# Kernel tuning notes

Hardware: AMD Instinct MI355X
Metric: run time of the kernel (lower is better)

Reference implementation:

```python
import jax, jax.numpy as jnp
import numpy as np

B, S, H = 2, 2048, 2048
N_HEADS, N_KV, HEAD_DIM = 16, 8, 128
EPS = 1e-6
ROPE_THETA = 1e6


def _rms_norm(x, w, eps=EPS):
    # per-head RMSNorm over last dim (head_dim), computed in fp32
    xf = x.astype(jnp.float32)
    var = jnp.mean(xf * xf, axis=-1, keepdims=True)
    return (w * (xf * jax.lax.rsqrt(var + eps))).astype(x.dtype)


def _rotate_half(x):
    x1, x2 = jnp.split(x, 2, axis=-1)
    return jnp.concatenate((-x2, x1), axis=-1)


def setup_inputs() -> dict:
    key = jax.random.key(0)
    ks = jax.random.split(key, 6)
    hidden_states = jax.random.normal(ks[0], (B, S, H), dtype=jnp.float32)
    # RoPE tables: [B, S, head_dim]
    inv_freq = 1.0 / (ROPE_THETA ** (np.arange(0, HEAD_DIM, 2, dtype=np.float32) / HEAD_DIM))
    pos = np.arange(S, dtype=np.float32)
    freqs = np.outer(pos, inv_freq)                      # [S, head_dim/2]
    emb = np.concatenate([freqs, freqs], axis=-1)        # [S, head_dim]
    cos = jnp.broadcast_to(jnp.asarray(np.cos(emb)), (B, S, HEAD_DIM))
    sin = jnp.broadcast_to(jnp.asarray(np.sin(emb)), (B, S, HEAD_DIM))
    # additive causal mask [B, 1, S, S]
    causal = jnp.triu(jnp.full((S, S), -1e9, dtype=jnp.float32), k=1)
    attention_mask = jnp.broadcast_to(causal[None, None], (B, 1, S, S))
    scale = 0.02
    Wq = jax.random.normal(ks[1], (N_HEADS * HEAD_DIM, H), dtype=jnp.float32) * scale
    Wk = jax.random.normal(ks[2], (N_KV * HEAD_DIM, H), dtype=jnp.float32) * scale
    Wv = jax.random.normal(ks[3], (N_KV * HEAD_DIM, H), dtype=jnp.float32) * scale
    Wo = jax.random.normal(ks[4], (H, N_HEADS * HEAD_DIM), dtype=jnp.float32) * scale
    q_norm_w = jnp.ones((HEAD_DIM,), dtype=jnp.float32)
    k_norm_w = jnp.ones((HEAD_DIM,), dtype=jnp.float32)
    return dict(hidden_states=hidden_states, cos=cos, sin=sin,
                attention_mask=attention_mask, Wq=Wq, Wk=Wk, Wv=Wv, Wo=Wo,
                q_norm_w=q_norm_w, k_norm_w=k_norm_w)


def reference(hidden_states, cos, sin, attention_mask, Wq, Wk, Wv, Wo, q_norm_w, k_norm_w):
    b, s, _ = hidden_states.shape
    scaling = HEAD_DIM ** -0.5
    n_rep = N_HEADS // N_KV
    # QKV projections (torch Linear: x @ W.T), split into heads
    q = jnp.einsum('bsh,dh->bsd', hidden_states, Wq).reshape(b, s, N_HEADS, HEAD_DIM)
    k = jnp.einsum('bsh,dh->bsd', hidden_states, Wk).reshape(b, s, N_KV, HEAD_DIM)
    v = jnp.einsum('bsh,dh->bsd', hidden_states, Wv).reshape(b, s, N_KV, HEAD_DIM)
    # per-head QK RMSNorm, then [B, H, S, D]
    q = _rms_norm(q, q_norm_w).transpose(0, 2, 1, 3)
    k = _rms_norm(k, k_norm_w).transpose(0, 2, 1, 3)
    v = v.transpose(0, 2, 1, 3)
    # RoPE (cos/sin unsqueezed over head dim)
    c = cos[:, None, :, :]
    sn = sin[:, None, :, :]
    q = q * c + _rotate_half(q) * sn
    k = k * c + _rotate_half(k) * sn
    # GQA: repeat kv heads
    k = jnp.repeat(k, n_rep, axis=1)
    v = jnp.repeat(v, n_rep, axis=1)
    # eager attention: materialize full [B, H, S, S] scores
    attn_weights = jnp.einsum('bhqd,bhkd->bhqk', q, k) * scaling + attention_mask
    attn_weights = jax.nn.softmax(attn_weights.astype(jnp.float32), axis=-1).astype(q.dtype)
    attn_output = jnp.einsum('bhqk,bhkd->bhqd', attn_weights, v)
    attn_output = attn_output.transpose(0, 2, 1, 3).reshape(b, s, N_HEADS * HEAD_DIM)
    attn_output = jnp.einsum('bsd,hd->bsh', attn_output, Wo)
    return attn_output, attn_weights
```

## Files before the change

### kernel.cpp

```cpp
#include <hip/hip_runtime.h>
#include <stdint.h>

typedef unsigned short u16;
typedef __attribute__((ext_vector_type(8))) short bf16x8;
typedef __attribute__((ext_vector_type(4))) float f32x4;
typedef __attribute__((ext_vector_type(8))) unsigned short u16x8;

#define SCALE_LOG2E 0.12751743007633614f

__device__ __forceinline__ u16 f2bf(float x){
  uint32_t u = __float_as_uint(x);
  u += 0x7FFFu + ((u >> 16) & 1u);
  return (u16)(u >> 16);
}
__device__ __forceinline__ float bf2f(u16 h){
  return __uint_as_float(((uint32_t)h) << 16);
}
__device__ __forceinline__ void gload16(const void* g, void* l){
  __builtin_amdgcn_global_load_lds((const __attribute__((address_space(1))) void*)g,
                                   (__attribute__((address_space(3))) void*)l, 16, 0, 0);
}

__global__ __launch_bounds__(256) void k_cvt5(
    const float* __restrict__ s0, u16* __restrict__ d0,
    const float* __restrict__ s1, u16* __restrict__ d1,
    const float* __restrict__ s2, u16* __restrict__ d2,
    const float* __restrict__ s3, u16* __restrict__ d3,
    const float* __restrict__ s4, u16* __restrict__ d4)
{
  int b = blockIdx.x;
  const float* s; u16* d; int off;
  if      (b < 8192)  { s=s0; d=d0; off=b; }
  else if (b < 12288) { s=s1; d=d1; off=b-8192; }
  else if (b < 14336) { s=s2; d=d2; off=b-12288; }
  else if (b < 16384) { s=s3; d=d3; off=b-14336; }
  else                { s=s4; d=d4; off=b-16384; }
  size_t i = ((size_t)off * 256 + threadIdx.x) * 4;
  float4 v = *(const float4*)(s + i);
  ushort4 o;
  o.x = f2bf(v.x); o.y = f2bf(v.y); o.z = f2bf(v.z); o.w = f2bf(v.w);
  *(ushort4*)(d + i) = o;
}

#define STAGE_UNIT(PTR, ROWOFF, BUF, TENS, KS, T1) do{ \
  _Pragma("unroll") \
  for(int jj=0;jj<2;jj++){ \
    int rs_ = wid*32 + jj*16 + (lane>>2); \
    int kp_ = (lane&3) ^ ((rs_>>1)&3); \
    gload16((PTR) + (size_t)((ROWOFF)+rs_)*K + (size_t)(T1)*64 + (KS)*32 + kp_*8, \
            &lds[BUF][TENS][KS][(wid*2+jj)*512]); \
  }}while(0)

#define FRAG(BASE, ROW) (*(const bf16x8*)((BASE) + (ROW)*32 + ((c_ ^ (((ROW)>>1)&3))<<3)))

__global__ __launch_bounds__(512,2) void k_gemm256(
    const u16* __restrict__ A, const u16* __restrict__ Bw, void* __restrict__ Cout,
    int N, int K, int ldc, int out_f32)
{
  __shared__ u16 lds[2][2][2][256*32];
  const int tid = threadIdx.x, wid = tid>>6, lane = tid&63;
  const int nbn = N >> 8;
  const int cpx = gridDim.x >> 3;
  const int bid = (blockIdx.x & 7)*cpx + (blockIdx.x >> 3);
  const int bm = bid / nbn, bn = bid % nbn;
  const int m0 = bm<<8, n0 = bn<<8;
  const int wm = wid>>2, wn = wid&3;
  const int c_ = lane>>4, rl = lane&15;

  f32x4 acc[8][4];
  f32x4 zero4 = {0.f,0.f,0.f,0.f};
#pragma unroll
  for (int i=0;i<8;i++)
#pragma unroll
    for (int j=0;j<4;j++) acc[i][j] = zero4;

  STAGE_UNIT(A,  m0, 0, 0, 0, 0);
  STAGE_UNIT(Bw, n0, 0, 1, 0, 0);
  STAGE_UNIT(A,  m0, 0, 0, 1, 0);
  STAGE_UNIT(Bw, n0, 0, 1, 1, 0);

  const int nt = K >> 6;
#pragma unroll 2
  for (int t=0; t<nt; ++t) {
    const int cur = t&1, nxt = cur^1;
    const bool pf = (t+1 < nt);
    const u16* Ab0 = lds[cur][0][0];
    const u16* Bb0 = lds[cur][1][0];
    const u16* Ab1 = lds[cur][0][1];
    const u16* Bb1 = lds[cur][1][1];
    bf16x8 af[4], bf[4];

    asm volatile("s_waitcnt vmcnt(4)" ::: "memory");
    __builtin_amdgcn_s_barrier();
    asm volatile("" ::: "memory");
#pragma unroll
    for (int j=0;j<4;j++) bf[j] = FRAG(Bb0, wn*64 + j*16 + rl);
#pragma unroll
    for (int i=0;i<4;i++) af[i] = FRAG(Ab0, wm*128 + i*16 + rl);
    if (pf) STAGE_UNIT(A, m0, nxt, 0, 0, t+1);
    __builtin_amdgcn_s_setprio(1);
#pragma unroll
    for (int i=0;i<4;i++)
#pragma unroll
      for (int j=0;j<4;j++)
        acc[i][j] = __builtin_amdgcn_mfma_f32_16x16x32_bf16(af[i], bf[j], acc[i][j], 0,0,0);
    __builtin_amdgcn_s_setprio(0);
    __builtin_amdgcn_s_barrier();
    asm volatile("" ::: "memory");

#pragma unroll
    for (int i=0;i<4;i++) af[i] = FRAG(Ab0, wm*128 + (i+4)*16 + rl);
    if (pf) STAGE_UNIT(Bw, n0, nxt, 1, 0, t+1);
    __builtin_amdgcn_s_setprio(1);
#pragma unroll
    for (int i=0;i<4;i++)
#pragma unroll
      for (int j=0;j<4;j++)
        acc[i+4][j] = __builtin_amdgcn_mfma_f32_16x16x32_bf16(af[i], bf[j], acc[i+4][j], 0,0,0);
    __builtin_amdgcn_s_setprio(0);
    __builtin_amdgcn_s_barrier();
    asm volatile("" ::: "memory");

    if (pf) { asm volatile("s_waitcnt vmcnt(4)" ::: "memory"); }
    else    { asm volatile("s_waitcnt vmcnt(0)" ::: "memory"); }
    __builtin_amdgcn_s_barrier();
    asm volatile("" ::: "memory");
#pragma unroll
    for (int j=0;j<4;j++) bf[j] = FRAG(Bb1, wn*64 + j*16 + rl);
#pragma unroll
    for (int i=0;i<4;i++) af[i] = FRAG(Ab1, wm*128 + i*16 + rl);
    if (pf) STAGE_UNIT(A, m0, nxt, 0, 1, t+1);
    __builtin_amdgcn_s_setprio(1);
#pragma unroll
    for (int i=0;i<4;i++)
#pragma unroll
      for (int j=0;j<4;j++)
        acc[i][j] = __builtin_amdgcn_mfma_f32_16x16x32_bf16(af[i], bf[j], acc[i][j], 0,0,0);
    __builtin_amdgcn_s_setprio(0);
    __builtin_amdgcn_s_barrier();
    asm volatile("" ::: "memory");

#pragma unroll
    for (int i=0;i<4;i++) af[i] = FRAG(Ab1, wm*128 + (i+4)*16 + rl);
    if (pf) STAGE_UNIT(Bw, n0, nxt, 1, 1, t+1);
    __builtin_amdgcn_s_setprio(1);
#pragma unroll
    for (int i=0;i<4;i++)
#pragma unroll
      for (int j=0;j<4;j++)
        acc[i+4][j] = __builtin_amdgcn_mfma_f32_16x16x32_bf16(af[i], bf[j], acc[i+4][j], 0,0,0);
    __builtin_amdgcn_s_setprio(0);
    __builtin_amdgcn_s_barrier();
    asm volatile("" ::: "memory");
  }

  const int r0 = m0 + wm*128 + ((lane>>4)<<2);
  const int c0 = n0 + wn*64 + rl;
  if (out_f32) {
    float* C = (float*)Cout;
#pragma unroll
    for (int i=0;i<8;i++)
#pragma unroll
      for (int j=0;j<4;j++)
#pragma unroll
        for (int r=0;r<4;r++)
          C[(size_t)(r0 + i*16 + r)*ldc + (c0 + j*16)] = acc[i][j][r];
  } else {
    u16* C = (u16*)Cout;
#pragma unroll
    for (int i=0;i<8;i++)
#pragma unroll
      for (int j=0;j<4;j++)
#pragma unroll
        for (int r=0;r<4;r++)
          C[(size_t)(r0 + i*16 + r)*ldc + (c0 + j*16)] = f2bf(acc[i][j][r]);
  }
}

__global__ __launch_bounds__(256) void k_normrope(
    u16* __restrict__ qkv, const float* __restrict__ cosb, const float* __restrict__ sinb,
    const float* __restrict__ qw, const float* __restrict__ kw)
{
  const int tid = threadIdx.x, lane = tid&63;
  const int task = blockIdx.x*4 + (tid>>6);
  int bs, col; const float* w;
  if (task < 65536) { bs = task >> 4; col = (task & 15)*128; w = qw; }
  else { int t2 = task - 65536; bs = t2 >> 3; col = 2048 + (t2 & 7)*128; w = kw; }
  u16* row = qkv + (size_t)bs*4096 + col;
  float x0 = bf2f(row[lane]), x1 = bf2f(row[lane+64]);
  float ss = x0*x0 + x1*x1;
#pragma unroll
  for (int m=1; m<64; m<<=1) ss += __shfl_xor(ss, m, 64);
  float rn = rsqrtf(ss*(1.0f/128.0f) + 1e-6f);
  const float* cp = cosb + (size_t)bs*128;
  const float* sp = sinb + (size_t)bs*128;
  float q0 = x0*rn*w[lane], q1 = x1*rn*w[lane+64];
  float o0 = q0*cp[lane]    - q1*sp[lane];
  float o1 = q1*cp[lane+64] + q0*sp[lane+64];
  row[lane]    = f2bf(o0);
  row[lane+64] = f2bf(o1);
}

__global__ __launch_bounds__(256) void k_vtrans(const u16* __restrict__ qkv, u16* __restrict__ vt)
{
  const int bid = blockIdx.x;
  const int dt = bid & 1, st = (bid>>1)&31, kvh = (bid>>6)&7, b = bid>>9;
  __shared__ u16 tile[64][72];
  const int tid = threadIdx.x;
  const int rr = tid >> 3, c = (tid & 7) * 8;
  const u16* src = qkv + ((size_t)(b*2048 + st*64))*4096 + 3072 + kvh*128 + dt*64;
#pragma unroll
  for (int p=0;p<2;p++){
    int sl = p*32 + rr;
    u16x8 v = *(const u16x8*)(src + (size_t)sl*4096 + c);
#pragma unroll
    for (int e=0;e<8;e++) tile[sl][c+e] = v[e];
  }
  __syncthreads();
  u16* dst = vt + ((size_t)((b*8+kvh)*128 + dt*64))*2048 + st*64;
#pragma unroll
  for (int p=0;p<2;p++){
    int dl = p*32 + rr;
    u16x8 o;
#pragma unroll
    for (int e=0;e<8;e++) o[e] = tile[c+e][dl];
    *(u16x8*)(dst + (size_t)dl*2048 + c) = o;
  }
}

#define STAGE_K(T, DSTBUF) do { \
  _Pragma("unroll") \
  for (int i_=0;i_<4;i_++){ \
    int r_ = wv*16 + i_*4 + (lane>>4); \
    int cs_ = (lane&15) ^ (r_&7); \
    gload16(Kb + (size_t)((T)*64 + r_)*4096 + cs_*8, (DSTBUF) + (wv*4+i_)*512); \
  } } while(0)

#define STAGE_V(T, DSTBUF) do { \
  _Pragma("unroll") \
  for (int i_=0;i_<4;i_++){ \
    int d_ = wv*32 + i_*8 + (lane>>3); \
    int cs_ = (lane&7) ^ (d_&7); \
    gload16(Vb + (size_t)d_*2048 + (T)*64 + cs_*8, (DSTBUF) + (wv*4+i_)*512); \
  } } while(0)

#define COMPUTE_S(SACC, KBUF) do { \
  _Pragma("unroll") \
  for (int ks_=0;ks_<4;ks_++){ \
    bf16x8 bfr_[4]; \
    _Pragma("unroll") \
    for (int ns_=0;ns_<4;ns_++){ \
      int n_ = ns_*16 + (lane&15); \
      int sl_ = (ks_*4 + (lane>>4)) ^ (n_&7); \
      bfr_[ns_] = *(const bf16x8*)((KBUF) + n_*128 + sl_*8); \
    } \
    _Pragma("unroll") \
    for (int ms_=0;ms_<2;ms_++) \
      _Pragma("unroll") \
      for (int ns_=0;ns_<4;ns_++) \
        SACC[ms_][ns_] = __builtin_amdgcn_mfma_f32_16x16x32_bf16(qf[ms_][ks_], bfr_[ns_], SACC[ms_][ns_], 0,0,0); \
  } } while(0)

__global__ __launch_bounds__(256) void k_attn(
    const u16* __restrict__ qkv, const u16* __restrict__ vt,
    float* __restrict__ probs, u16* __restrict__ attn_o)
{
  __shared__ u16 lK[2][64*128];
  __shared__ u16 lV[2][128*64];
  __shared__ u16 lP[4][32*64];
  const int tid = threadIdx.x, wv = tid>>6, lane = tid&63;
  const int bid = blockIdx.x;
  const int r9 = bid >> 5;
  const int qt = (r9 < 8) ? (15 - r9) : (r9 - 8);
  const int bh = bid & 31;
  const int h = bh & 15, b = bh >> 4;
  const int kvh = h>>1;
  const int q0 = qt<<7;
  const u16* Qb = qkv + (size_t)b*2048*4096 + h*128;
  const u16* Kb = qkv + (size_t)b*2048*4096 + 2048 + kvh*128;
  const u16* Vb = vt + (size_t)(b*8+kvh)*128*2048;

  f32x4 zero4 = {0.f,0.f,0.f,0.f};

  bf16x8 qf[2][4];
#pragma unroll
  for (int ms=0;ms<2;ms++)
#pragma unroll
    for (int ks=0;ks<4;ks++){
      int r = q0 + wv*32 + ms*16 + (lane&15);
      int cc = ks*32 + (lane>>4)*8;
      qf[ms][ks] = *(const bf16x8*)(Qb + (size_t)r*4096 + cc);
    }

  const int nkt = 2*qt + 2;
  float lsum[2][4];
#pragma unroll
  for (int ms=0;ms<2;ms++)
#pragma unroll
    for (int r=0;r<4;r++) lsum[ms][r] = 0.f;

  int cur = 0;
  STAGE_K(0, lK[0]);
  asm volatile("s_waitcnt vmcnt(0)" ::: "memory");
  __syncthreads();
  for (int t=0; t<nkt; ++t) {
    if (t+1 < nkt) STAGE_K(t+1, lK[cur^1]);
    f32x4 sacc[2][4];
#pragma unroll
    for (int ms=0;ms<2;ms++)
#pragma unroll
      for (int ns=0;ns<4;ns++) sacc[ms][ns] = zero4;
    COMPUTE_S(sacc, lK[cur]);
    const int rb = q0 + wv*32 + ((lane>>4)<<2);
    const int cb = t*64 + (lane&15);
#pragma unroll
    for (int ms=0;ms<2;ms++)
#pragma unroll
      for (int ns=0;ns<4;ns++)
#pragma unroll
        for (int r=0;r<4;r++){
          int rg = rb + ms*16 + r, cg = cb + ns*16;
          float e = __builtin_exp2f(sacc[ms][ns][r]*SCALE_LOG2E);
          lsum[ms][r] += (cg <= rg) ? e : 0.f;
        }
    asm volatile("s_waitcnt vmcnt(0)" ::: "memory");
    __syncthreads();
    cur ^= 1;
  }
#pragma unroll
  for (int m=1;m<16;m<<=1)
#pragma unroll
    for (int ms=0;ms<2;ms++)
#pragma unroll
      for (int r=0;r<4;r++) lsum[ms][r] += __shfl_xor(lsum[ms][r], m, 64);
  float linv[2][4];
#pragma unroll
  for (int ms=0;ms<2;ms++)
#pragma unroll
    for (int r=0;r<4;r++) linv[ms][r] = 1.0f / lsum[ms][r];

  f32x4 oacc[2][8];
#pragma unroll
  for (int ms=0;ms<2;ms++)
#pragma unroll
    for (int nd=0;nd<8;nd++) oacc[ms][nd] = zero4;

  u16* pw = lP[wv];
  float* pb = probs + (size_t)(b*16+h)*2048*2048;

  cur = 0;
  STAGE_K(0, lK[0]);
  STAGE_V(0, lV[0]);
  asm volatile("s_waitcnt vmcnt(0)" ::: "memory");
  __syncthreads();
  for (int t=0; t<nkt; ++t) {
    if (t+1 < nkt) { STAGE_K(t+1, lK[cur^1]); STAGE_V(t+1, lV[cur^1]); }
    asm volatile("" ::: "memory");
    f32x4 sacc[2][4];
#pragma unroll
    for (int ms=0;ms<2;ms++)
#pragma unroll
      for (int ns=0;ns<4;ns++) sacc[ms][ns] = zero4;
    COMPUTE_S(sacc, lK[cur]);
    const int rb = q0 + wv*32 + ((lane>>4)<<2);
    const int cb = t*64 + (lane&15);
#pragma unroll
    for (int ms=0;ms<2;ms++)
#pragma unroll
      for (int ns=0;ns<4;ns++)
#pragma unroll
        for (int r=0;r<4;r++){
          int rg = rb + ms*16 + r, cg = cb + ns*16;
          float p = (cg <= rg) ? __builtin_exp2f(sacc[ms][ns][r]*SCALE_LOG2E)*linv[ms][r] : 0.f;
          __builtin_nontemporal_store(p, pb + (size_t)rg*2048 + cg);
          int ql = ms*16 + ((lane>>4)<<2) + r;
          int kl = ns*16 + (lane&15);
          pw[ql*64 + (((kl>>3) ^ (ql&7))<<3) + (kl&7)] = f2bf(p);
        }
    const u16* vbuf = lV[cur];
#pragma unroll
    for (int kks=0;kks<2;kks++){
      bf16x8 pa[2];
#pragma unroll
      for (int ms=0;ms<2;ms++){
        int ql = ms*16 + (lane&15);
        int sl = (kks*4 + (lane>>4)) ^ (ql&7);
        pa[ms] = *(const bf16x8*)(pw + ql*64 + sl*8);
      }
#pragma unroll
      for (int nd=0;nd<8;nd++){
        int d = nd*16 + (lane&15);
        int sl = (kks*4 + (lane>>4)) ^ (d&7);
        bf16x8 vb = *(const bf16x8*)(vbuf + d*64 + sl*8);
#pragma unroll
        for (int ms=0;ms<2;ms++)
          oacc[ms][nd] = __builtin_amdgcn_mfma_f32_16x16x32_bf16(pa[ms], vb, oacc[ms][nd], 0,0,0);
      }
    }
    if (t+1 < nkt) {
      asm volatile("s_waitcnt vmcnt(32)" ::: "memory");
      __syncthreads();
    }
    cur ^= 1;
  }

  const int kend = nkt*64;
  f32x4 z4 = {0.f,0.f,0.f,0.f};
  for (int q = wv*32; q < wv*32+32; ++q){
    float* rp = pb + (size_t)(q0 + q)*2048;
    for (int c = kend + lane*4; c < 2048; c += 256)
      __builtin_nontemporal_store(z4, (f32x4*)(rp + c));
  }

#pragma unroll
  for (int ms=0;ms<2;ms++)
#pragma unroll
    for (int nd=0;nd<8;nd++)
#pragma unroll
      for (int r=0;r<4;r++){
        int rg = q0 + wv*32 + ms*16 + ((lane>>4)<<2) + r;
        int cg = h*128 + nd*16 + (lane&15);
        attn_o[(size_t)(b*2048 + rg)*2048 + cg] = f2bf(oacc[ms][nd][r]);
      }
}

extern "C" void kernel_launch(void* const* d_in, const int* in_sizes, int n_in,
                              void* d_out, int out_size, void* d_ws, size_t ws_size,
                              hipStream_t stream) {
  (void)in_sizes; (void)n_in; (void)out_size; (void)ws_size;
  const float* hs   = (const float*)d_in[0];
  const float* cosb = (const float*)d_in[1];
  const float* sinb = (const float*)d_in[2];
  const float* Wq   = (const float*)d_in[4];
  const float* Wk   = (const float*)d_in[5];
  const float* Wv   = (const float*)d_in[6];
  const float* Wo   = (const float*)d_in[7];
  const float* qw   = (const float*)d_in[8];
  const float* kw   = (const float*)d_in[9];
  float* out   = (float*)d_out;
  float* probs = out + 8388608;

  char* ws = (char*)d_ws;
  u16* hs_b   = (u16*)(ws);
  u16* attn_o = hs_b;
  u16* W_all  = (u16*)(ws + (16u<<20));
  u16* Wo_b   = (u16*)(ws + (32u<<20));
  u16* qkv    = (u16*)(ws + (40u<<20));
  u16* v_t    = (u16*)(ws + (72u<<20));

  k_cvt5<<<20480,256,0,stream>>>(hs, hs_b, Wq, W_all, Wk, W_all + 4194304,
                                 Wv, W_all + 6291456, Wo, Wo_b);

  k_gemm256<<<256,512,0,stream>>>(hs_b, W_all, (void*)qkv, 4096, 2048, 4096, 0);
  k_normrope<<<24576,256,0,stream>>>(qkv, cosb, sinb, qw, kw);
  k_vtrans<<<1024,256,0,stream>>>(qkv, v_t);
  k_attn<<<512,256,0,stream>>>(qkv, v_t, probs, attn_o);
  k_gemm256<<<128,512,0,stream>>>(attn_o, Wo_b, (void*)out, 2048, 2048, 2048, 1);
}
```

Measured before the change: 388.9 us.

## Skip fully masked tiles per wave, swap MFMA operands, single-buffer V

Each wave now skips QK^T and PV work for key tiles past its own causal diagonal, and applies the mask only on the diagonal tile. The S MFMA operands are swapped so each lane holds four consecutive key columns of one query row. That allows vectorized float4 nontemporal stores of probabilities, a cheaper row-sum reduction, and packed bf16 writes to LDS. V is staged into a single LDS buffer each iteration with finer-grained vmcnt waits and an extra barrier, and s_setprio is placed around the MFMA bursts. This lowers LDS use and cuts wasted compute, at the cost of more synchronisation and less prefetch depth for V.

```diff
diff --git a/kernel.cpp b/kernel.cpp
--- a/kernel.cpp
+++ b/kernel.cpp
@@ -4,6 +4,7 @@
 typedef unsigned short u16;
 typedef __attribute__((ext_vector_type(8))) short bf16x8;
 typedef __attribute__((ext_vector_type(4))) float f32x4;
+typedef __attribute__((ext_vector_type(4))) unsigned short u16x4;
 typedef __attribute__((ext_vector_type(8))) unsigned short u16x8;
 
 #define SCALE_LOG2E 0.12751743007633614f
@@ -244,21 +245,23 @@
     gload16(Vb + (size_t)d_*2048 + (T)*64 + cs_*8, (DSTBUF) + (wv*4+i_)*512); \
   } } while(0)
 
-#define COMPUTE_S(SACC, KBUF) do { \
+#define COMPUTE_S_SW(SACC, KBUF) do { \
   _Pragma("unroll") \
   for (int ks_=0;ks_<4;ks_++){ \
-    bf16x8 bfr_[4]; \
+    bf16x8 kfr_[4]; \
     _Pragma("unroll") \
     for (int ns_=0;ns_<4;ns_++){ \
       int n_ = ns_*16 + (lane&15); \
       int sl_ = (ks_*4 + (lane>>4)) ^ (n_&7); \
-      bfr_[ns_] = *(const bf16x8*)((KBUF) + n_*128 + sl_*8); \
+      kfr_[ns_] = *(const bf16x8*)((KBUF) + n_*128 + sl_*8); \
     } \
+    __builtin_amdgcn_s_setprio(1); \
     _Pragma("unroll") \
     for (int ms_=0;ms_<2;ms_++) \
       _Pragma("unroll") \
       for (int ns_=0;ns_<4;ns_++) \
-        SACC[ms_][ns_] = __builtin_amdgcn_mfma_f32_16x16x32_bf16(qf[ms_][ks_], bfr_[ns_], SACC[ms_][ns_], 0,0,0); \
+        SACC[ms_][ns_] = __builtin_amdgcn_mfma_f32_16x16x32_bf16(kfr_[ns_], qf[ms_][ks_], SACC[ms_][ns_], 0,0,0); \
+    __builtin_amdgcn_s_setprio(0); \
   } } while(0)
 
 __global__ __launch_bounds__(256) void k_attn(
@@ -266,9 +269,10 @@
     float* __restrict__ probs, u16* __restrict__ attn_o)
 {
   __shared__ u16 lK[2][64*128];
-  __shared__ u16 lV[2][128*64];
+  __shared__ u16 lV[128*64];
   __shared__ u16 lP[4][32*64];
   const int tid = threadIdx.x, wv = tid>>6, lane = tid&63;
+  const int rl = lane&15, hi = lane>>4;
   const int bid = blockIdx.x;
   const int r9 = bid >> 5;
   const int qt = (r9 < 8) ? (15 - r9) : (r9 - 8);
@@ -287,17 +291,16 @@
   for (int ms=0;ms<2;ms++)
 #pragma unroll
     for (int ks=0;ks<4;ks++){
-      int r = q0 + wv*32 + ms*16 + (lane&15);
-      int cc = ks*32 + (lane>>4)*8;
+      int r = q0 + wv*32 + ms*16 + rl;
+      int cc = ks*32 + hi*8;
       qf[ms][ks] = *(const bf16x8*)(Qb + (size_t)r*4096 + cc);
     }
 
   const int nkt = 2*qt + 2;
-  float lsum[2][4];
-#pragma unroll
-  for (int ms=0;ms<2;ms++)
-#pragma unroll
-    for (int r=0;r<4;r++) lsum[ms][r] = 0.f;
+  const int tdiag = 2*qt + (wv>>1);
+  const int rg0 = q0 + wv*32 + rl;
+
+  float lsum[2] = {0.f, 0.f};
 
   int cur = 0;
   STAGE_K(0, lK[0]);
@@ -305,39 +308,51 @@
   __syncthreads();
   for (int t=0; t<nkt; ++t) {
     if (t+1 < nkt) STAGE_K(t+1, lK[cur^1]);
-    f32x4 sacc[2][4];
-#pragma unroll
-    for (int ms=0;ms<2;ms++)
-#pragma unroll
-      for (int ns=0;ns<4;ns++) sacc[ms][ns] = zero4;
-    COMPUTE_S(sacc, lK[cur]);
-    const int rb = q0 + wv*32 + ((lane>>4)<<2);
-    const int cb = t*64 + (lane&15);
-#pragma unroll
-    for (int ms=0;ms<2;ms++)
-#pragma unroll
-      for (int ns=0;ns<4;ns++)
-#pragma unroll
-        for (int r=0;r<4;r++){
-          int rg = rb + ms*16 + r, cg = cb + ns*16;
-          float e = __builtin_exp2f(sacc[ms][ns][r]*SCALE_LOG2E);
-          lsum[ms][r] += (cg <= rg) ? e : 0.f;
+    asm volatile("" ::: "memory");
+    if (t <= tdiag) {
+      f32x4 sacc[2][4];
+#pragma unroll
+      for (int ms=0;ms<2;ms++)
+#pragma unroll
+        for (int ns=0;ns<4;ns++) sacc[ms][ns] = zero4;
+      COMPUTE_S_SW(sacc, lK[cur]);
+      if (t == tdiag) {
+#pragma unroll
+        for (int ms=0;ms<2;ms++){
+          const int rg = rg0 + ms*16;
+#pragma unroll
+          for (int ns=0;ns<4;ns++){
+            const int cg0 = t*64 + ns*16 + hi*4;
+#pragma unroll
+            for (int r=0;r<4;r++){
+              float e = __builtin_exp2f(sacc[ms][ns][r]*SCALE_LOG2E);
+              lsum[ms] += (cg0 + r <= rg) ? e : 0.f;
+            }
+          }
         }
+      } else {
+#pragma unroll
+        for (int ms=0;ms<2;ms++)
+#pragma unroll
+          for (int ns=0;ns<4;ns++){
+            float e0 = __builtin_exp2f(sacc[ms][ns][0]*SCALE_LOG2E);
+            float e1 = __builtin_exp2f(sacc[ms][ns][1]*SCALE_LOG2E);
+            float e2 = __builtin_exp2f(sacc[ms][ns][2]*SCALE_LOG2E);
+            float e3 = __builtin_exp2f(sacc[ms][ns][3]*SCALE_LOG2E);
+            lsum[ms] += (e0+e1)+(e2+e3);
+          }
+      }
+    }
     asm volatile("s_waitcnt vmcnt(0)" ::: "memory");
     __syncthreads();
     cur ^= 1;
   }
 #pragma unroll
-  for (int m=1;m<16;m<<=1)
-#pragma unroll
-    for (int ms=0;ms<2;ms++)
-#pragma unroll
-      for (int r=0;r<4;r++) lsum[ms][r] += __shfl_xor(lsum[ms][r], m, 64);
-  float linv[2][4];
-#pragma unroll
-  for (int ms=0;ms<2;ms++)
-#pragma unroll
-    for (int r=0;r<4;r++) linv[ms][r] = 1.0f / lsum[ms][r];
+  for (int ms=0;ms<2;ms++){
+    lsum[ms] += __shfl_xor(lsum[ms], 16, 64);
+    lsum[ms] += __shfl_xor(lsum[ms], 32, 64);
+  }
+  float linv[2] = {1.0f/lsum[0], 1.0f/lsum[1]};
 
   f32x4 oacc[2][8];
 #pragma unroll
@@ -350,61 +365,84 @@
 
   cur = 0;
   STAGE_K(0, lK[0]);
-  STAGE_V(0, lV[0]);
   asm volatile("s_waitcnt vmcnt(0)" ::: "memory");
   __syncthreads();
   for (int t=0; t<nkt; ++t) {
-    if (t+1 < nkt) { STAGE_K(t+1, lK[cur^1]); STAGE_V(t+1, lV[cur^1]); }
-    asm volatile("" ::: "memory");
-    f32x4 sacc[2][4];
-#pragma unroll
-    for (int ms=0;ms<2;ms++)
-#pragma unroll
-      for (int ns=0;ns<4;ns++) sacc[ms][ns] = zero4;
-    COMPUTE_S(sacc, lK[cur]);
-    const int rb = q0 + wv*32 + ((lane>>4)<<2);
-    const int cb = t*64 + (lane&15);
-#pragma unroll
-    for (int ms=0;ms<2;ms++)
-#pragma unroll
-      for (int ns=0;ns<4;ns++)
-#pragma unroll
-        for (int r=0;r<4;r++){
-          int rg = rb + ms*16 + r, cg = cb + ns*16;
-          float p = (cg <= rg) ? __builtin_exp2f(sacc[ms][ns][r]*SCALE_LOG2E)*linv[ms][r] : 0.f;
-          __builtin_nontemporal_store(p, pb + (size_t)rg*2048 + cg);
-          int ql = ms*16 + ((lane>>4)<<2) + r;
-          int kl = ns*16 + (lane&15);
-          pw[ql*64 + (((kl>>3) ^ (ql&7))<<3) + (kl&7)] = f2bf(p);
+    const bool pf = (t+1 < nkt);
+    STAGE_V(t, lV);
+    if (pf) STAGE_K(t+1, lK[cur^1]);
+    asm volatile("" ::: "memory");
+    if (t <= tdiag) {
+      f32x4 sacc[2][4];
+#pragma unroll
+      for (int ms=0;ms<2;ms++)
+#pragma unroll
+        for (int ns=0;ns<4;ns++) sacc[ms][ns] = zero4;
+      COMPUTE_S_SW(sacc, lK[cur]);
+      const int cb = t*64;
+#pragma unroll
+      for (int ms=0;ms<2;ms++){
+        const int rg = rg0 + ms*16;
+        float* prow = pb + (size_t)rg*2048 + cb + hi*4;
+        const int lrow = ms*16 + rl;
+#pragma unroll
+        for (int ns=0;ns<4;ns++){
+          f32x4 pv;
+          if (t == tdiag) {
+            const int cg0 = cb + ns*16 + hi*4;
+#pragma unroll
+            for (int r=0;r<4;r++){
+              float e = __builtin_exp2f(sacc[ms][ns][r]*SCALE_LOG2E)*linv[ms];
+              pv[r] = (cg0 + r <= rg) ? e : 0.f;
+            }
+          } else {
+#pragma unroll
+            for (int r=0;r<4;r++)
+              pv[r] = __builtin_exp2f(sacc[ms][ns][r]*SCALE_LOG2E)*linv[ms];
+          }
+          __builtin_nontemporal_store(pv, (f32x4*)(prow + ns*16));
+          u16x4 pk;
+#pragma unroll
+          for (int r=0;r<4;r++) pk[r] = f2bf(pv[r]);
+          const int sp = (ns*4 + hi) ^ ((rl&7)<<1);
+          *(u16x4*)(pw + lrow*64 + sp*4) = pk;
         }
-    const u16* vbuf = lV[cur];
-#pragma unroll
-    for (int kks=0;kks<2;kks++){
-      bf16x8 pa[2];
-#pragma unroll
-      for (int ms=0;ms<2;ms++){
-        int ql = ms*16 + (lane&15);
-        int sl = (kks*4 + (lane>>4)) ^ (ql&7);
-        pa[ms] = *(const bf16x8*)(pw + ql*64 + sl*8);
-      }
-#pragma unroll
-      for (int nd=0;nd<8;nd++){
-        int d = nd*16 + (lane&15);
-        int sl = (kks*4 + (lane>>4)) ^ (d&7);
-        bf16x8 vb = *(const bf16x8*)(vbuf + d*64 + sl*8);
-#pragma unroll
-        for (int ms=0;ms<2;ms++)
-          oacc[ms][nd] = __builtin_amdgcn_mfma_f32_16x16x32_bf16(pa[ms], vb, oacc[ms][nd], 0,0,0);
       }
     }
-    if (t+1 < nkt) {
-      asm volatile("s_waitcnt vmcnt(32)" ::: "memory");
+    if (pf) { asm volatile("s_waitcnt vmcnt(12)" ::: "memory"); }
+    else    { asm volatile("s_waitcnt vmcnt(0)"  ::: "memory"); }
+    __syncthreads();
+    if (t <= tdiag) {
+#pragma unroll
+      for (int kks=0;kks<2;kks++){
+        bf16x8 pa[2];
+#pragma unroll
+        for (int ms=0;ms<2;ms++){
+          const int lrow = ms*16 + rl;
+          const int sp = (kks*8 + 2*hi) ^ ((rl&7)<<1);
+          pa[ms] = *(const bf16x8*)(pw + lrow*64 + sp*4);
+        }
+#pragma unroll
+        for (int nd=0;nd<8;nd++){
+          const int d = nd*16 + rl;
+          const int sl = (kks*4 + hi) ^ (d&7);
+          bf16x8 vb = *(const bf16x8*)(lV + d*64 + sl*8);
+          __builtin_amdgcn_s_setprio(1);
+#pragma unroll
+          for (int ms=0;ms<2;ms++)
+            oacc[ms][nd] = __builtin_amdgcn_mfma_f32_16x16x32_bf16(pa[ms], vb, oacc[ms][nd], 0,0,0);
+          __builtin_amdgcn_s_setprio(0);
+        }
+      }
+    }
+    if (pf) {
+      asm volatile("s_waitcnt vmcnt(8)" ::: "memory");
       __syncthreads();
     }
     cur ^= 1;
   }
 
-  const int kend = nkt*64;
+  const int kend = (tdiag+1)*64;
   f32x4 z4 = {0.f,0.f,0.f,0.f};
   for (int q = wv*32; q < wv*32+32; ++q){
     float* rp = pb + (size_t)(q0 + q)*2048;
@@ -418,8 +456,8 @@
     for (int nd=0;nd<8;nd++)
 #pragma unroll
       for (int r=0;r<4;r++){
-        int rg = q0 + wv*32 + ms*16 + ((lane>>4)<<2) + r;
-        int cg = h*128 + nd*16 + (lane&15);
+        int rg = q0 + wv*32 + ms*16 + hi*4 + r;
+        int cg = h*128 + nd*16 + rl;
         attn_o[(size_t)(b*2048 + rg)*2048 + cg] = f2bf(oacc[ms][nd][r]);
       }
 }
```

Result: slower. 423.8 us (+9.0%).
